# Performance work log

Hardware: AMD Instinct MI355X
Metric: run time of the kernel (lower is better)

Reference implementation:

```python
import jax, jax.numpy as jnp
import numpy as np

B, T, S, R, L = 16, 32, 512, 8, 256
H, E, V, NL = 512, 512, 50000, 3
OOV = 50


def setup_inputs() -> dict:
    key = jax.random.key(0)
    ks = jax.random.split(key, 40)
    p = lambda i, shape: jax.random.normal(ks[i], shape, dtype=jnp.float32) * 0.02
    d = {
        'tokens': jax.random.randint(ks[0], (B, T), 0, V),
        'src_oov': jax.random.randint(ks[1], (B, S), 0, V),
        'ref_oovs': jax.random.randint(ks[2], (B, R, L), 0, V),
        'src_mask': jnp.ones((B, S), bool),
        'ref_word_mask': jnp.ones((B, R, L), bool),
        'ref_doc_mask': jnp.ones((B, R), bool),
        'max_num_oov': OOV,
        'cur_word_rep': jax.random.normal(ks[3], (B, S, H), dtype=jnp.float32),
        'ref_word_reps': jax.random.normal(ks[4], (B, R, L, H), dtype=jnp.float32),
        'ref_doc_reps': jax.random.normal(ks[5], (B, R, H), dtype=jnp.float32),
        'hidden0': jax.random.normal(ks[6], (NL, B, H), dtype=jnp.float32),
        'embed_w': p(7, (V, E)),
        'gru_wih': p(8, (NL, 3 * H, H)),  # layer0 input dim E == H
        'gru_whh': p(9, (NL, 3 * H, H)),
        'gru_bih': p(10, (NL, 3 * H)),
        'gru_bhh': p(11, (NL, 3 * H)),
        'attn_Wd': p(12, (H, H)), 'attn_We': p(13, (H, H)), 'attn_v': p(14, (H,)),
        'hd_Wd': p(15, (H, H)), 'hd_We': p(16, (H, H)), 'hd_v': p(17, (H,)),
        'hw_Wd': p(18, (H, H)), 'hw_We': p(19, (H, H)), 'hw_v': p(20, (H,)),
        'gate_w': p(21, (2 * H, 1)), 'gate_b': p(22, (1,)),
        'fc_w': p(23, (2 * H, H)), 'fc_b': p(24, (H,)),
        'out_w': p(25, (H, V)), 'out_b': p(26, (V,)),
        'pgen_w': p(27, (E + 2 * H, 3)), 'pgen_b': p(28, (3,)),
    }
    return d


def _forward(embed_w, gru_wih, gru_whh, gru_bih, gru_bhh,
             attn_Wd, attn_We, attn_v, hd_Wd, hd_We, hd_v, hw_Wd, hw_We, hw_v,
             gate_w, gate_b, fc_w, fc_b, out_w, out_b, pgen_w, pgen_b,
             cur_word_rep, ref_word_reps, ref_doc_reps, hidden0,
             tokens, src_oov, ref_oovs, src_mask, ref_word_mask, ref_doc_mask,
             max_num_oov):
    b, t = tokens.shape
    x = embed_w[tokens]                               # [B,T,E]
    enc_proj = cur_word_rep @ attn_We                 # [B,S,H]
    doc_proj = ref_doc_reps @ hd_We                   # [B,R,H]
    word_proj = ref_word_reps @ hw_We                 # [B,R,L,H]
    NEG = jnp.float32(-1e9)

    def step(hidden, x_t):
        inp = x_t
        hs = []
        for l in range(hidden.shape[0]):
            gx = inp @ gru_wih[l].T + gru_bih[l]
            gh = hidden[l] @ gru_whh[l].T + gru_bhh[l]
            xr, xz, xn = jnp.split(gx, 3, -1)
            hr, hz, hn = jnp.split(gh, 3, -1)
            r = jax.nn.sigmoid(xr + hr)
            z = jax.nn.sigmoid(xz + hz)
            n = jnp.tanh(xn + r * hn)
            h = (1.0 - z) * n + z * hidden[l]
            hs.append(h)
            inp = h
        new_hidden = jnp.stack(hs)
        h_top = hs[-1]                                # [B,H]
        # additive attention over source words
        sc = jnp.tanh(enc_proj + (h_top @ attn_Wd)[:, None, :]) @ attn_v  # [B,S]
        aw = jax.nn.softmax(jnp.where(src_mask, sc, NEG), -1)
        ctx = jnp.einsum('bs,bsh->bh', aw, cur_word_rep)
        # hierarchical attention: doc level then word level
        scd = jnp.tanh(doc_proj + (h_top @ hd_Wd)[:, None, :]) @ hd_v     # [B,R]
        ad = jax.nn.softmax(jnp.where(ref_doc_mask, scd, NEG), -1)
        scw = jnp.tanh(word_proj + (h_top @ hw_Wd)[:, None, None, :]) @ hw_v  # [B,R,L]
        aww = jax.nn.softmax(jnp.where(ref_word_mask, scw, NEG), -1)
        ra = ad[:, :, None] * aww                     # [B,R,L]
        rctx = jnp.einsum('brl,brlh->bh', ra, ref_word_reps)
        # fusion gate
        g = jax.nn.sigmoid(jnp.concatenate([ctx, rctx], -1) @ gate_w + gate_b)  # [B,1]
        context = g * ctx + (1.0 - g) * rctx
        return new_hidden, (context, h_top, aw, ra)

    _, (contexts, hiddens, attn_dists, ref_attn_dists) = jax.lax.scan(
        step, hidden0, jnp.swapaxes(x, 0, 1))
    contexts = jnp.swapaxes(contexts, 0, 1)           # [B,T,H]
    hiddens = jnp.swapaxes(hiddens, 0, 1)             # [B,T,H]
    attn_dists = jnp.swapaxes(attn_dists, 0, 1)       # [B,T,S]
    ref_attn_dists = jnp.swapaxes(ref_attn_dists, 0, 1)  # [B,T,R,L]

    ch = jnp.concatenate([contexts, hiddens], -1)
    vocab_dist = jax.nn.softmax((ch @ fc_w + fc_b) @ out_w + out_b, -1)  # [B,T,V]
    pg = jax.nn.softmax(jnp.concatenate([contexts, hiddens, x], -1) @ pgen_w + pgen_b, -1)  # [B,T,3]
    vocab_dist_ = pg[..., 0:1] * vocab_dist
    attn_ = pg[..., 1:2] * attn_dists
    final = jnp.concatenate(
        [vocab_dist_, jnp.zeros((b, t, max_num_oov), vocab_dist_.dtype)], -1)
    bi = jnp.arange(b)[:, None, None]
    ti = jnp.arange(t)[None, :, None]
    idx = jnp.broadcast_to(src_oov[:, None, :], (b, t, src_oov.shape[-1]))
    final = final.at[bi, ti, idx].add(attn_)
    # multi-doc copy
    r, l = ref_oovs.shape[1], ref_oovs.shape[2]
    ref_attn_ = pg[..., 2][:, :, None, None] * ref_attn_dists
    ridx = jnp.broadcast_to(ref_oovs.reshape(b, 1, r * l), (b, t, r * l))
    final = final.at[bi, ti, ridx].add(ref_attn_.reshape(b, t, r * l))
    return final, attn_dists


def reference(tokens, src_oov, ref_oovs, src_mask, ref_word_mask, ref_doc_mask,
              max_num_oov, cur_word_rep, ref_word_reps, ref_doc_reps, hidden0,
              embed_w, gru_wih, gru_whh, gru_bih, gru_bhh,
              attn_Wd, attn_We, attn_v, hd_Wd, hd_We, hd_v, hw_Wd, hw_We, hw_v,
              gate_w, gate_b, fc_w, fc_b, out_w, out_b, pgen_w, pgen_b):
    return _forward(embed_w, gru_wih, gru_whh, gru_bih, gru_bhh,
                    attn_Wd, attn_We, attn_v, hd_Wd, hd_We, hd_v,
                    hw_Wd, hw_We, hw_v, gate_w, gate_b, fc_w, fc_b,
                    out_w, out_b, pgen_w, pgen_b,
                    cur_word_rep, ref_word_reps, ref_doc_reps, hidden0,
                    tokens, src_oov, ref_oovs, src_mask, ref_word_mask,
                    ref_doc_mask, max_num_oov)
```

## Files before the change

kernel.cpp:

```cpp
#include <hip/hip_runtime.h>
#include <hip/hip_bf16.h>


#define B_   16
#define T_   32
#define S_   512
#define R_   8
#define L_   256
#define RL_  2048
#define H_   512
#define V_   50000
#define NL_  3
#define OOV_ 50
#define M_   512
#define FINW 50050
#define S2C  2.8853900817779268f
#define GRUB 128
#define NCONV 128
#define HP16 520

typedef __attribute__((ext_vector_type(8))) short    short8;
typedef __attribute__((ext_vector_type(4))) float    f32x4;
typedef __attribute__((ext_vector_type(2))) _Float16 h2;
typedef __attribute__((ext_vector_type(8))) _Float16 h8;
typedef unsigned short u16;
typedef unsigned int   u32;
typedef unsigned long long u64;

#if __has_builtin(__builtin_amdgcn_exp2f)
#define EXP2F __builtin_amdgcn_exp2f
#else
#define EXP2F exp2f
#endif
#if __has_builtin(__builtin_amdgcn_rcpf)
#define RCPF __builtin_amdgcn_rcpf
#else
#define RCPF(x) (1.f/(x))
#endif

__device__ __forceinline__ float bf2f(u16 u){
  union { u32 i; float f; } v; v.i = ((u32)u) << 16; return v.f;
}
__device__ __forceinline__ u16 f2bf(float f){
  union { float f; u32 i; } v; v.f = f;
  return (u16)((v.i + 0x7FFFu + ((v.i >> 16) & 1u)) >> 16);
}
__device__ __forceinline__ u16 f2h(float f){
  union { _Float16 h; u16 u; } v; v.h = (_Float16)f; return v.u;
}
__device__ __forceinline__ float tanh_(float x){
  float e = __expf(2.f * x);
  return 1.f - 2.f / (e + 1.f);
}
__device__ __forceinline__ float sigmoid_(float x){
  return 1.f / (1.f + __expf(-x));
}
__device__ __forceinline__ float dot8h(h8 w, h8 x, float acc){
#if __has_builtin(__builtin_amdgcn_fdot2)
  acc = __builtin_amdgcn_fdot2((h2){w[0], w[1]}, (h2){x[0], x[1]}, acc, false);
  acc = __builtin_amdgcn_fdot2((h2){w[2], w[3]}, (h2){x[2], x[3]}, acc, false);
  acc = __builtin_amdgcn_fdot2((h2){w[4], w[5]}, (h2){x[4], x[5]}, acc, false);
  acc = __builtin_amdgcn_fdot2((h2){w[6], w[7]}, (h2){x[6], x[7]}, acc, false);
#else
  #pragma unroll
  for (int q = 0; q < 8; q++) acc += (float)w[q] * (float)x[q];
#endif
  return acc;
}
__device__ __forceinline__ u64 allc(const u64* p){
  return __hip_atomic_load(p, __ATOMIC_RELAXED, __HIP_MEMORY_SCOPE_AGENT);
}
__device__ __forceinline__ float allcf(const float* p){
  u32 v = __hip_atomic_load((const u32*)p, __ATOMIC_RELAXED, __HIP_MEMORY_SCOPE_AGENT);
  union { u32 i; float f; } c; c.i = v; return c.f;
}


__global__ __launch_bounds__(256) void k_embed(const int* __restrict__ tokens,
                                               const float* __restrict__ embed_w,
                                               u16* __restrict__ x_bf){
  int rid = blockIdx.x;
  long tok = (long)tokens[rid];
  const float* src = embed_w + tok * H_;
  u16* dst = x_bf + (long)rid * H_;
  for (int e = threadIdx.x; e < H_; e += 256) dst[e] = f2bf(src[e]);
}

struct CJ { const float* s; u16* d; long n; int f16; };

__global__ __launch_bounds__(256) void k_conv6(CJ j0, CJ j1, CJ j2, CJ j3, CJ j4, CJ j5){
  int y = blockIdx.y;
  CJ j = (y == 0) ? j0 : (y == 1) ? j1 : (y == 2) ? j2 : (y == 3) ? j3 : (y == 4) ? j4 : j5;
  long n4 = j.n >> 2;
  long i = (long)blockIdx.x * 256 + threadIdx.x;
  long stride = (long)gridDim.x * 256;
  if (j.f16){
    for (; i < n4; i += stride){
      f32x4 v = *(const f32x4*)(j.s + 4 * i);
      u64 p = (u64)f2h(v[0]) | ((u64)f2h(v[1]) << 16)
            | ((u64)f2h(v[2]) << 32) | ((u64)f2h(v[3]) << 48);
      *(u64*)(j.d + 4 * i) = p;
    }
  } else {
    for (; i < n4; i += stride){
      f32x4 v = *(const f32x4*)(j.s + 4 * i);
      u64 p = (u64)f2bf(v[0]) | ((u64)f2bf(v[1]) << 16)
            | ((u64)f2bf(v[2]) << 32) | ((u64)f2bf(v[3]) << 48);
      *(u64*)(j.d + 4 * i) = p;
    }
  }
}

__global__ __launch_bounds__(256) void k_convT(const float* __restrict__ src, int Rr, int Cc,
                                               u16* __restrict__ dst){
  __shared__ float tile[32][33];
  int c0 = blockIdx.x * 32, r0 = blockIdx.y * 32;
  int tx = threadIdx.x & 31, ty = threadIdx.x >> 5;
  for (int i = ty; i < 32; i += 8){
    int r = r0 + i, c = c0 + tx;
    tile[i][tx] = (r < Rr && c < Cc) ? src[(long)r * Cc + c] : 0.f;
  }
  __syncthreads();
  for (int i = ty; i < 32; i += 8){
    int c = c0 + i, r = r0 + tx;
    if (c < Cc && r < Rr) dst[(long)c * Rr + r] = f2bf(tile[tx][i]);
  }
}

__global__ __launch_bounds__(256) void k_convT6(const float* s0, const float* s1,
    const float* s2, const float* s3, const float* s4, const float* s5,
    u16* __restrict__ dstb){
  int z = blockIdx.z;
  const float* src = (z == 0) ? s0 : (z == 1) ? s1 : (z == 2) ? s2
                   : (z == 3) ? s3 : (z == 4) ? s4 : s5;
  u16* dst = dstb + (long)z * H_ * H_;
  __shared__ float tile[32][33];
  int c0 = blockIdx.x * 32, r0 = blockIdx.y * 32;
  int tx = threadIdx.x & 31, ty = threadIdx.x >> 5;
  for (int i = ty; i < 32; i += 8)
    tile[i][tx] = src[(long)(r0 + i) * H_ + c0 + tx];
  __syncthreads();
  for (int i = ty; i < 32; i += 8)
    dst[(long)(c0 + i) * H_ + r0 + tx] = f2bf(tile[tx][i]);
}


__device__ void dev_gemm_tile(const u16* __restrict__ A, int lda,
                              const u16* __restrict__ W, int ldw,
                              const float* __restrict__ bias,
                              void* __restrict__ Cv, long ldc,
                              int N, int K, int c_bf16, float cscale,
                              int bx, int by, int t256){
  int wave = t256 >> 6, lane = t256 & 63;
  int m0 = bx * 128 + (wave >> 1) * 64;
  int n0 = by * 128 + (wave & 1) * 64;
  int lr = lane & 15, lk = (lane >> 4) * 8;
  f32x4 acc[4][4];
  #pragma unroll
  for (int i = 0; i < 4; i++)
    #pragma unroll
    for (int j = 0; j < 4; j++) acc[i][j] = (f32x4){0.f, 0.f, 0.f, 0.f};

  short8 a0[4], b0[4];
  #pragma unroll
  for (int i = 0; i < 4; i++)
    a0[i] = *(const short8*)(A + (long)(m0 + i * 16 + lr) * lda + lk);
  #pragma unroll
  for (int j = 0; j < 4; j++){
    int c = n0 + j * 16 + lr;
    b0[j] = (c < N) ? *(const short8*)(W + (long)c * ldw + lk) : (short8){0,0,0,0,0,0,0,0};
  }
  for (int k0 = 0; k0 < K; k0 += 32){
    short8 a1[4], b1[4];
    if (k0 + 32 < K){
      int kn = k0 + 32 + lk;
      #pragma unroll
      for (int i = 0; i < 4; i++)
        a1[i] = *(const short8*)(A + (long)(m0 + i * 16 + lr) * lda + kn);
      #pragma unroll
      for (int j = 0; j < 4; j++){
        int c = n0 + j * 16 + lr;
        b1[j] = (c < N) ? *(const short8*)(W + (long)c * ldw + kn) : (short8){0,0,0,0,0,0,0,0};
      }
    }
    #pragma unroll
    for (int i = 0; i < 4; i++)
      #pragma unroll
      for (int j = 0; j < 4; j++)
        acc[i][j] = __builtin_amdgcn_mfma_f32_16x16x32_bf16(a0[i], b0[j], acc[i][j], 0, 0, 0);
    #pragma unroll
    for (int i = 0; i < 4; i++) a0[i] = a1[i];
    #pragma unroll
    for (int j = 0; j < 4; j++) b0[j] = b1[j];
  }
  int rr = (lane >> 4) * 4;
  #pragma unroll
  for (int j = 0; j < 4; j++){
    int c = n0 + j * 16 + lr;
    if (c >= N) continue;
    float bv = bias ? bias[c] : 0.f;
    #pragma unroll
    for (int i = 0; i < 4; i++){
      #pragma unroll
      for (int e = 0; e < 4; e++){
        long r = m0 + i * 16 + rr + e;
        float v = fmaf(acc[i][j][e], cscale, bv);
        if (c_bf16) ((u16*)Cv)[r * ldc + c] = f2bf(v);
        else        ((float*)Cv)[r * ldc + c] = v;
      }
    }
  }
}

__global__ __launch_bounds__(256) void k_gemm_nt(const u16* __restrict__ A, int lda,
                                                 const u16* __restrict__ W, int ldw,
                                                 const float* __restrict__ bias,
                                                 void* __restrict__ Cv, long ldc,
                                                 int N, int K, int c_bf16, float cscale){
  dev_gemm_tile(A, lda, W, ldw, bias, Cv, ldc, N, K, c_bf16, cscale,
                blockIdx.x, blockIdx.y, threadIdx.x);
}


__global__ __launch_bounds__(256) void k_gemm_out(const u16* __restrict__ A,
    const u16* __restrict__ W, const float* __restrict__ bias,
    float* __restrict__ fin, float* __restrict__ pm, float* __restrict__ ps){
  const int N = V_;
  __shared__ float cbuf[128][132];
  __shared__ float smx[128][2], ssx[128][2];
  int tid = threadIdx.x;
  int wave = tid >> 6, lane = tid & 63;
  int mb = blockIdx.x * 128, nb = blockIdx.y * 128;
  int m0 = mb + (wave >> 1) * 64;
  int n0 = nb + (wave & 1) * 64;
  int lr = lane & 15, lk = (lane >> 4) * 8;
  f32x4 acc[4][4];
  #pragma unroll
  for (int i = 0; i < 4; i++)
    #pragma unroll
    for (int j = 0; j < 4; j++) acc[i][j] = (f32x4){0.f, 0.f, 0.f, 0.f};

  short8 a0[4], b0[4];
  #pragma unroll
  for (int i = 0; i < 4; i++)
    a0[i] = *(const short8*)(A + (long)(m0 + i * 16 + lr) * 512 + lk);
  #pragma unroll
  for (int j = 0; j < 4; j++){
    int c = n0 + j * 16 + lr;
    b0[j] = (c < N) ? *(const short8*)(W + (long)c * 512 + lk) : (short8){0,0,0,0,0,0,0,0};
  }
  for (int k0 = 0; k0 < 512; k0 += 32){
    short8 a1[4], b1[4];
    if (k0 + 32 < 512){
      int kn = k0 + 32 + lk;
      #pragma unroll
      for (int i = 0; i < 4; i++)
        a1[i] = *(const short8*)(A + (long)(m0 + i * 16 + lr) * 512 + kn);
      #pragma unroll
      for (int j = 0; j < 4; j++){
        int c = n0 + j * 16 + lr;
        b1[j] = (c < N) ? *(const short8*)(W + (long)c * 512 + kn) : (short8){0,0,0,0,0,0,0,0};
      }
    }
    #pragma unroll
    for (int i = 0; i < 4; i++)
      #pragma unroll
      for (int j = 0; j < 4; j++)
        acc[i][j] = __builtin_amdgcn_mfma_f32_16x16x32_bf16(a0[i], b0[j], acc[i][j], 0, 0, 0);
    #pragma unroll
    for (int i = 0; i < 4; i++) a0[i] = a1[i];
    #pragma unroll
    for (int j = 0; j < 4; j++) b0[j] = b1[j];
  }
  int rr = (lane >> 4) * 4;
  int rloc0 = (wave >> 1) * 64, cloc0 = (wave & 1) * 64;
  #pragma unroll
  for (int j = 0; j < 4; j++){
    int c = n0 + j * 16 + lr;
    float bv = (c < N) ? bias[c] : 0.f;
    #pragma unroll
    for (int i = 0; i < 4; i++){
      #pragma unroll
      for (int e = 0; e < 4; e++)
        cbuf[rloc0 + i * 16 + rr + e][cloc0 + j * 16 + lr] = acc[i][j][e] + bv;
    }
  }
  __syncthreads();
  int rl = tid >> 1, ch = tid & 1;
  int cbase = ch * 64;
  int cg = nb + cbase;
  long gbase = (long)(mb + rl) * FINW + cg;
  float mp = -1e30f;
  #pragma unroll 8
  for (int k = 0; k < 64; k += 2){
    float x0 = cbuf[rl][cbase + k], x1 = cbuf[rl][cbase + k + 1];
    float2 xy; xy.x = x0; xy.y = x1;
    *(float2*)(fin + gbase + k) = xy;
    if (cg + k < N)     mp = fmaxf(mp, x0);
    if (cg + k + 1 < N) mp = fmaxf(mp, x1);
  }
  float sp = 0.f;
  #pragma unroll 8
  for (int k = 0; k < 64; k++){
    if (cg + k < N) sp += __expf(cbuf[rl][cbase + k] - mp);
  }
  smx[rl][ch] = mp; ssx[rl][ch] = sp;
  __syncthreads();
  if (tid < 128){
    float ma = smx[tid][0], mb2 = smx[tid][1];
    float M = fmaxf(ma, mb2);
    float S = ssx[tid][0] * __expf(ma - M) + ssx[tid][1] * __expf(mb2 - M);
    long row = mb + tid;
    pm[row * 392 + blockIdx.y] = M;
    ps[row * 392 + blockIdx.y] = S;
  }
}


__global__ __launch_bounds__(512) void k_gru_mega(
    const float* __restrict__ gx0, const u16* __restrict__ wih_h,
    const u16* __restrict__ whh_h, const float* __restrict__ bih,
    const float* __restrict__ bhh, const float* __restrict__ hidden0,
    float* __restrict__ h_all, u16* __restrict__ ch_bf, unsigned int* cnt,
    const float* __restrict__ out_w, u16* __restrict__ outwT,
    const u16* __restrict__ cwr_bf, const u16* __restrict__ rwr_bf,
    const u16* __restrict__ rdr_bf, const u16* __restrict__ WT,
    u16* __restrict__ enc_bf, u16* __restrict__ wp_bf,
    float* __restrict__ doc_proj, int do_shadow){
  __shared__ u16 pH0[16][HP16], pH1[16][HP16], pX1[16][HP16], pH2[16][HP16], pX2[16][HP16];
  __shared__ float red0[8][3][4][16];
  __shared__ float red1[8][6][4][16];
  __shared__ float red2[8][6][4][16];
  __shared__ float tconv[2][32][33];
  int bid = blockIdx.x;
  int tid = threadIdx.x;

  if (bid >= GRUB){
    if (!do_shadow) return;
    int wid = bid - GRUB;
    int half = tid >> 8, t256 = tid & 255;
    int worker = wid * 2 + half;
    for (int tile = worker; tile < 1284; tile += 256){
      if (tile < 256)
        dev_gemm_tile(cwr_bf, H_, WT, H_, (const float*)0, (void*)enc_bf, H_,
                      H_, H_, 1, S2C, tile >> 2, tile & 3, t256);
      else if (tile < 1280){
        int t = tile - 256;
        dev_gemm_tile(rwr_bf, H_, WT + 2 * H_ * H_, H_, (const float*)0, (void*)wp_bf, H_,
                      H_, H_, 1, S2C, t >> 2, t & 3, t256);
      } else
        dev_gemm_tile(rdr_bf, H_, WT + H_ * H_, H_, (const float*)0, (void*)doc_proj, H_,
                      H_, H_, 0, S2C, 0, tile - 1280, t256);
    }
    __syncthreads();
    int sub = half, tx = t256 & 31, ty = t256 >> 5;
    const int NT = 1563 * 16;
    for (int base = wid * 2; base < NT; base += NCONV * 2){
      int tile = base + sub;
      bool act = tile < NT;
      int cx = act ? (tile % 1563) : 0;
      int ry = act ? (tile / 1563) : 0;
      int c0 = cx * 32, r0 = ry * 32;
      if (act){
        for (int i = ty; i < 32; i += 8){
          int c = c0 + tx;
          tconv[sub][i][tx] = (c < V_) ? out_w[(long)(r0 + i) * V_ + c] : 0.f;
        }
      }
      __syncthreads();
      if (act){
        for (int i = ty; i < 32; i += 8){
          int c = c0 + i;
          if (c < V_) outwT[(long)c * H_ + r0 + tx] = f2bf(tconv[sub][tx][i]);
        }
      }
      __syncthreads();
    }
    return;
  }

  int bx = bid;
  int b = tid & 15, jj = (tid >> 4) & 3, ks = tid >> 6;
  int j = bx * 4 + jj;
  int kbase = ks * 64;
  int srow = tid >> 5, sl32 = tid & 31;

  for (int s = 0; s < T_ + NL_ - 1; s++){
    int t0 = s, t1 = s - 1, t2v = s - 2;
    bool a0 = (t0 < T_);
    bool a1 = (t1 >= 0 && t1 < T_);
    bool a2 = (t2v >= 0 && t2v < T_);
    float hpj_r = 0.f, gx_r0 = 0.f, gx_r1 = 0.f, gx_r2 = 0.f;
    if (tid < 192){
      int lz = tid >> 6, b2 = tid & 15, jj2 = (tid >> 4) & 3;
      int j2 = bx * 4 + jj2;
      int tt = s - lz;
      if (tt >= 0 && tt < T_){
        hpj_r = (tt == 0) ? hidden0[(lz * B_ + b2) * H_ + j2]
                          : allcf(h_all + (long)((lz * T_ + tt - 1) * B_ + b2) * H_ + j2);
        if (lz == 0){
          const float* g = gx0 + (long)(b2 * T_ + tt) * 1536 + j2;
          gx_r0 = g[0]; gx_r1 = g[512]; gx_r2 = g[1024];
        }
      }
    }
    {
      u64 v;
      #define STAGE(PAN, ROWPTR, ATOMIC)                                         \
        {                                                                        \
          const u64* p = (const u64*)(ROWPTR);                                   \
          _Pragma("unroll")                                                      \
          for (int q = 0; q < 8; q++){                                           \
            v = (ATOMIC) ? allc(p + sl32 + 32 * q) : p[sl32 + 32 * q];           \
            union { u64 w; float f[2]; } uu; uu.w = v;                           \
            union { _Float16 h[2]; u32 u; } pk;                                  \
            pk.h[0] = (_Float16)uu.f[0]; pk.h[1] = (_Float16)uu.f[1];            \
            *(u32*)&PAN[srow][2 * (sl32 + 32 * q)] = pk.u;                       \
          }                                                                      \
        }
      if (a0){
        if (t0 == 0) STAGE(pH0, hidden0 + (long)(0 * B_ + srow) * H_, false)
        else         STAGE(pH0, h_all + (long)((0 * T_ + t0 - 1) * B_ + srow) * H_, true)
      }
      if (a1){
        if (t1 == 0) STAGE(pH1, hidden0 + (long)(1 * B_ + srow) * H_, false)
        else         STAGE(pH1, h_all + (long)((1 * T_ + t1 - 1) * B_ + srow) * H_, true)
        STAGE(pX1, h_all + (long)((0 * T_ + t1) * B_ + srow) * H_, true)
      }
      if (a2){
        if (t2v == 0) STAGE(pH2, hidden0 + (long)(2 * B_ + srow) * H_, false)
        else          STAGE(pH2, h_all + (long)((2 * T_ + t2v - 1) * B_ + srow) * H_, true)
        STAGE(pX2, h_all + (long)((1 * T_ + t2v) * B_ + srow) * H_, true)
      }
      #undef STAGE
    }
    __syncthreads();

    if (a0){
      const u16* wl = whh_h;
      const h8* w0 = (const h8*)(wl + ((long)(0 * H_ + j)) * H_ + kbase);
      const h8* w1 = (const h8*)(wl + ((long)(1 * H_ + j)) * H_ + kbase);
      const h8* w2 = (const h8*)(wl + ((long)(2 * H_ + j)) * H_ + kbase);
      float s0 = 0.f, s1 = 0.f, s2 = 0.f;
      #pragma unroll 2
      for (int k8 = 0; k8 < 8; k8++){
        h8 hv = *(const h8*)&pH0[b][kbase + 8 * k8];
        s0 = dot8h(w0[k8], hv, s0);
        s1 = dot8h(w1[k8], hv, s1);
        s2 = dot8h(w2[k8], hv, s2);
      }
      red0[ks][0][jj][b] = s0; red0[ks][1][jj][b] = s1; red0[ks][2][jj][b] = s2;
    }
    if (a1){
      const u16* wl = whh_h + (long)1 * 1536 * H_;
      const u16* ul = wih_h + (long)1 * 1536 * H_;
      const h8* w0 = (const h8*)(wl + ((long)(0 * H_ + j)) * H_ + kbase);
      const h8* w1 = (const h8*)(wl + ((long)(1 * H_ + j)) * H_ + kbase);
      const h8* w2 = (const h8*)(wl + ((long)(2 * H_ + j)) * H_ + kbase);
      const h8* u0 = (const h8*)(ul + ((long)(0 * H_ + j)) * H_ + kbase);
      const h8* u1 = (const h8*)(ul + ((long)(1 * H_ + j)) * H_ + kbase);
      const h8* u2 = (const h8*)(ul + ((long)(2 * H_ + j)) * H_ + kbase);
      float s0 = 0.f, s1 = 0.f, s2 = 0.f, x0 = 0.f, x1 = 0.f, x2 = 0.f;
      #pragma unroll 2
      for (int k8 = 0; k8 < 8; k8++){
        h8 hv = *(const h8*)&pH1[b][kbase + 8 * k8];
        h8 xv = *(const h8*)&pX1[b][kbase + 8 * k8];
        s0 = dot8h(w0[k8], hv, s0);
        s1 = dot8h(w1[k8], hv, s1);
        s2 = dot8h(w2[k8], hv, s2);
        x0 = dot8h(u0[k8], xv, x0);
        x1 = dot8h(u1[k8], xv, x1);
        x2 = dot8h(u2[k8], xv, x2);
      }
      red1[ks][0][jj][b] = s0; red1[ks][1][jj][b] = s1; red1[ks][2][jj][b] = s2;
      red1[ks][3][jj][b] = x0; red1[ks][4][jj][b] = x1; red1[ks][5][jj][b] = x2;
    }
    if (a2){
      const u16* wl = whh_h + (long)2 * 1536 * H_;
      const u16* ul = wih_h + (long)2 * 1536 * H_;
      const h8* w0 = (const h8*)(wl + ((long)(0 * H_ + j)) * H_ + kbase);
      const h8* w1 = (const h8*)(wl + ((long)(1 * H_ + j)) * H_ + kbase);
      const h8* w2 = (const h8*)(wl + ((long)(2 * H_ + j)) * H_ + kbase);
      const h8* u0 = (const h8*)(ul + ((long)(0 * H_ + j)) * H_ + kbase);
      const h8* u1 = (const h8*)(ul + ((long)(1 * H_ + j)) * H_ + kbase);
      const h8* u2 = (const h8*)(ul + ((long)(2 * H_ + j)) * H_ + kbase);
      float s0 = 0.f, s1 = 0.f, s2 = 0.f, x0 = 0.f, x1 = 0.f, x2 = 0.f;
      #pragma unroll 2
      for (int k8 = 0; k8 < 8; k8++){
        h8 hv = *(const h8*)&pH2[b][kbase + 8 * k8];
        h8 xv = *(const h8*)&pX2[b][kbase + 8 * k8];
        s0 = dot8h(w0[k8], hv, s0);
        s1 = dot8h(w1[k8], hv, s1);
        s2 = dot8h(w2[k8], hv, s2);
        x0 = dot8h(u0[k8], xv, x0);
        x1 = dot8h(u1[k8], xv, x1);
        x2 = dot8h(u2[k8], xv, x2);
      }
      red2[ks][0][jj][b] = s0; red2[ks][1][jj][b] = s1; red2[ks][2][jj][b] = s2;
      red2[ks][3][jj][b] = x0; red2[ks][4][jj][b] = x1; red2[ks][5][jj][b] = x2;
    }
    __syncthreads();

    if (tid < 192){
      int lz = tid >> 6, b2 = tid & 15, jj2 = (tid >> 4) & 3;
      int j2 = bx * 4 + jj2;
      int tt = s - lz;
      if (tt >= 0 && tt < T_){
        float gh[3], gxv[3];
        #pragma unroll
        for (int g = 0; g < 3; g++){
          float a = 0.f, c = 0.f;
          if (lz == 0){
            #pragma unroll
            for (int q = 0; q < 8; q++) a += red0[q][g][jj2][b2];
          } else if (lz == 1){
            #pragma unroll
            for (int q = 0; q < 8; q++){ a += red1[q][g][jj2][b2]; c += red1[q][3 + g][jj2][b2]; }
          } else {
            #pragma unroll
            for (int q = 0; q < 8; q++){ a += red2[q][g][jj2][b2]; c += red2[q][3 + g][jj2][b2]; }
          }
          gh[g] = a + bhh[lz * 1536 + g * H_ + j2];
          if (lz == 0) gxv[g] = (g == 0) ? gx_r0 : (g == 1) ? gx_r1 : gx_r2;
          else         gxv[g] = c + bih[lz * 1536 + g * H_ + j2];
        }
        float r = sigmoid_(gxv[0] + gh[0]);
        float z = sigmoid_(gxv[1] + gh[1]);
        float n = tanh_(gxv[2] + r * gh[2]);
        float h = (1.f - z) * n + z * hpj_r;
        union { float f; u32 u; } cv; cv.f = h;
        __hip_atomic_store((u32*)(h_all + (long)((lz * T_ + tt) * B_ + b2) * H_ + j2),
                           cv.u, __ATOMIC_RELAXED, __HIP_MEMORY_SCOPE_AGENT);
        if (lz == 2) ch_bf[(long)(b2 * T_ + tt) * 1024 + 512 + j2] = f2bf(h);
      }
    }
    if (s == T_ + NL_ - 2) break;

    __syncthreads();
    if (tid == 0)
      __hip_atomic_store(cnt + bx * 16, (u32)(s + 1),
                         __ATOMIC_RELAXED, __HIP_MEMORY_SCOPE_AGENT);
    if (tid < GRUB){
      long guard = 0;
      while (__hip_atomic_load(cnt + tid * 16, __ATOMIC_RELAXED, __HIP_MEMORY_SCOPE_AGENT)
               < (u32)(s + 1) && guard < (1L << 23)){
        __builtin_amdgcn_s_sleep(1);
        guard++;
      }
    }
    __syncthreads();
  }
}


__global__ __launch_bounds__(256) void k_scores2(const u16* __restrict__ enc,
    const u16* __restrict__ wp, const float* __restrict__ dec_all,
    const float* __restrict__ av, const float* __restrict__ wv,
    float* __restrict__ aw, float* __restrict__ ra){
  int b = blockIdx.x, y = blockIdx.y, tz = blockIdx.z;
  const u16* ebf; int erpb, doff, et, ldo; const float* vv; float* out;
  if (y < 8){ ebf = enc; erpb = S_;  doff = 0;    vv = av; out = aw; ldo = S_;  et = y; }
  else      { ebf = wp;  erpb = RL_; doff = 1024; vv = wv; out = ra; ldo = RL_; et = y - 8; }
  int tid = threadIdx.x;
  __shared__ float dsh[8][512];
  __shared__ float vsh[512];
  __shared__ float redsv[4];
  for (int i = tid; i < 8 * 128; i += 256){
    int tl = i >> 7, c = (i & 127) << 2;
    *(f32x4*)&dsh[tl][c] =
      *(const f32x4*)(dec_all + ((long)(b * T_) + tz * 8 + tl) * 1536 + doff + c);
  }
  for (int i = tid; i < 128; i += 256)
    *(f32x4*)&vsh[i << 2] = *(const f32x4*)(vv + (i << 2));
  __syncthreads();
  float pvv = vsh[tid] + vsh[tid + 256];
  for (int o = 32; o > 0; o >>= 1) pvv += __shfl_xor(pvv, o);
  if ((tid & 63) == 0) redsv[tid >> 6] = pvv;
  __syncthreads();
  float sumv = redsv[0] + redsv[1] + redsv[2] + redsv[3];

  int el = tid & 63, tq = tid >> 6;
  const u16* erow = ebf + ((long)b * erpb + et * 64 + el) * H_;
  float acc0 = 0.f, acc1 = 0.f;
  for (int h0 = 0; h0 < H_; h0 += 8){
    short8 ev = *(const short8*)(erow + h0);
    float w[8], vq[8];
    #pragma unroll
    for (int q = 0; q < 8; q++) w[q] = bf2f((u16)ev[q]);
    #pragma unroll
    for (int q = 0; q < 8; q++) vq[q] = vsh[h0 + q];
    const float* d0 = &dsh[tq * 2 + 0][h0];
    const float* d1 = &dsh[tq * 2 + 1][h0];
    #pragma unroll
    for (int q = 0; q < 8; q++){
      float e0 = EXP2F(w[q] + d0[q]);
      acc0 += vq[q] * RCPF(e0 + 1.f);
      float e1 = EXP2F(w[q] + d1[q]);
      acc1 += vq[q] * RCPF(e1 + 1.f);
    }
  }
  int eg = et * 64 + el;
  long r0 = (long)(b * T_ + tz * 8 + tq * 2 + 0) * ldo + eg;
  long r1 = (long)(b * T_ + tz * 8 + tq * 2 + 1) * ldo + eg;
  out[r0] = sumv - 2.f * acc0;
  out[r1] = sumv - 2.f * acc1;
}


__global__ __launch_bounds__(256) void k_smax_scd(float* __restrict__ aw,
    const float* __restrict__ doc_proj, const float* __restrict__ dec_all,
    const float* __restrict__ hd_v, float* __restrict__ ad){
  int rid = blockIdx.x, tid = threadIdx.x;
  __shared__ float red4[4];
  __shared__ float red8[8][32];
  if (blockIdx.y == 0){
    float* row = aw + (long)rid * S_;
    float x0 = row[tid], x1 = row[tid + 256];
    float m = fmaxf(x0, x1);
    for (int o = 32; o > 0; o >>= 1) m = fmaxf(m, __shfl_xor(m, o));
    if ((tid & 63) == 0) red4[tid >> 6] = m;
    __syncthreads();
    m = fmaxf(fmaxf(red4[0], red4[1]), fmaxf(red4[2], red4[3]));
    float e0 = __expf(x0 - m), e1 = __expf(x1 - m);
    float s = e0 + e1;
    for (int o = 32; o > 0; o >>= 1) s += __shfl_xor(s, o);
    __syncthreads();
    if ((tid & 63) == 0) red4[tid >> 6] = s;
    __syncthreads();
    s = red4[0] + red4[1] + red4[2] + red4[3];
    float inv = 1.f / s;
    row[tid] = e0 * inv; row[tid + 256] = e1 * inv;
  } else {
    int b = rid / T_;
    int r = tid >> 5, kp = tid & 31;
    const float* dp = doc_proj + (long)(b * R_ + r) * H_;
    const float* d  = dec_all + (long)rid * 1536 + 512;
    float s = 0.f;
    for (int h = kp * 16; h < kp * 16 + 16; h++){
      float e = EXP2F(dp[h] + d[h]);
      s += hd_v[h] * (1.f - 2.f * RCPF(e + 1.f));
    }
    red8[r][kp] = s;
    __syncthreads();
    if (tid < 8){
      float sc = 0.f;
      for (int k = 0; k < 32; k++) sc += red8[tid][k];
      red8[tid][0] = sc;
    }
    __syncthreads();
    if (tid == 0){
      float m = -1e30f;
      for (int q = 0; q < 8; q++) m = fmaxf(m, red8[q][0]);
      float e[8], sum = 0.f;
      for (int q = 0; q < 8; q++){ e[q] = __expf(red8[q][0] - m); sum += e[q]; }
      float inv = 1.f / sum;
      for (int q = 0; q < 8; q++) ad[rid * R_ + q] = e[q] * inv;
    }
  }
}

__global__ __launch_bounds__(256) void k_aww_ra(float* __restrict__ raBuf,
                                                const float* __restrict__ ad){
  int rid = blockIdx.x, r = blockIdx.y, tid = threadIdx.x;
  float* row = raBuf + (long)rid * RL_ + r * L_;
  float x = row[tid];
  float m = x;
  for (int o = 32; o > 0; o >>= 1) m = fmaxf(m, __shfl_xor(m, o));
  __shared__ float red[4];
  if ((tid & 63) == 0) red[tid >> 6] = m;
  __syncthreads();
  m = fmaxf(fmaxf(red[0], red[1]), fmaxf(red[2], red[3]));
  float e = __expf(x - m);
  float s = e;
  for (int o = 32; o > 0; o >>= 1) s += __shfl_xor(s, o);
  __syncthreads();
  if ((tid & 63) == 0) red[tid >> 6] = s;
  __syncthreads();
  s = red[0] + red[1] + red[2] + red[3];
  row[tid] = (e / s) * ad[rid * R_ + r];
}


__global__ __launch_bounds__(256) void k_awgemm(const float* __restrict__ wts, int KS, int CH,
    const u16* __restrict__ Wbuf, float* __restrict__ pdst){
  int b = blockIdx.x, ht = blockIdx.y, kc = blockIdx.z;
  int tid = threadIdx.x;
  int hl = tid & 63, tq = tid >> 6;
  int h = ht * 256 + hl * 4;
  int base = kc * CH;
  float a[8][4];
  #pragma unroll
  for (int tt = 0; tt < 8; tt++)
    #pragma unroll
    for (int q = 0; q < 4; q++) a[tt][q] = 0.f;
  const float* wrow = wts + ((long)(b * T_) + tq * 8) * KS + base;
  for (int sl = 0; sl < CH; sl++){
    const u16* wp = Wbuf + ((long)b * KS + base + sl) * H_ + h;
    u32 p0 = *(const u32*)(wp);
    u32 p1 = *(const u32*)(wp + 2);
    float v0 = bf2f((u16)(p0 & 0xffff)), v1 = bf2f((u16)(p0 >> 16));
    float v2 = bf2f((u16)(p1 & 0xffff)), v3 = bf2f((u16)(p1 >> 16));
    #pragma unroll
    for (int tt = 0; tt < 8; tt++){
      float w = wrow[(long)tt * KS + sl];
      a[tt][0] += w * v0; a[tt][1] += w * v1;
      a[tt][2] += w * v2; a[tt][3] += w * v3;
    }
  }
  #pragma unroll
  for (int tt = 0; tt < 8; tt++){
    long o = (long)kc * (2 * M_ * H_) + ((long)(b * T_ + tq * 8 + tt)) * H_ + h;
    *(f32x4*)(pdst + o) = (f32x4){a[tt][0], a[tt][1], a[tt][2], a[tt][3]};
  }
}

__global__ __launch_bounds__(256) void k_red8(const float* __restrict__ pbuf,
                                              float* __restrict__ outp){
  long n = 2L * M_ * H_;
  long i = (long)blockIdx.x * 256 + threadIdx.x;
  if (i >= n) return;
  float s = 0.f;
  #pragma unroll
  for (int kc = 0; kc < 8; kc++) s += pbuf[(long)kc * n + i];
  outp[i] = s;
}


__global__ __launch_bounds__(256) void k_gatepgen(const float* __restrict__ ctx,
    const float* __restrict__ rctx, const float* __restrict__ gate_w,
    const float* __restrict__ gate_b, float* __restrict__ contexts,
    u16* __restrict__ ch_bf, const float* __restrict__ h_all,
    const u16* __restrict__ x_bf, const float* __restrict__ pgen_w,
    const float* __restrict__ pgen_b, float* __restrict__ pg){
  int rid = blockIdx.x, tid = threadIdx.x;
  int b = rid / T_, t = rid % T_;
  const float* c  = ctx  + (long)rid * H_;
  const float* rc = rctx + (long)rid * H_;
  float part = 0.f;
  for (int h = tid; h < H_; h += 256) part += c[h] * gate_w[h] + rc[h] * gate_w[H_ + h];
  for (int o = 32; o > 0; o >>= 1) part += __shfl_xor(part, o);
  __shared__ float red[4];
  if ((tid & 63) == 0) red[tid >> 6] = part;
  __syncthreads();
  float g = sigmoid_(red[0] + red[1] + red[2] + red[3] + gate_b[0]);
  for (int h = tid; h < H_; h += 256){
    float v = g * c[h] + (1.f - g) * rc[h];
    contexts[(long)rid * H_ + h] = v;
    ch_bf[(long)rid * 1024 + h] = f2bf(v);
  }
  float p0 = 0.f, p1 = 0.f, p2 = 0.f;
  for (int k = tid; k < 1536; k += 256){
    float v;
    if (k < 512)       v = g * c[k] + (1.f - g) * rc[k];
    else if (k < 1024) v = h_all[((2 * T_ + t) * B_ + b) * H_ + (k - 512)];
    else               v = bf2f(x_bf[(long)rid * H_ + (k - 1024)]);
    p0 += v * pgen_w[k * 3 + 0];
    p1 += v * pgen_w[k * 3 + 1];
    p2 += v * pgen_w[k * 3 + 2];
  }
  for (int o = 32; o > 0; o >>= 1){
    p0 += __shfl_xor(p0, o); p1 += __shfl_xor(p1, o); p2 += __shfl_xor(p2, o);
  }
  __shared__ float r0[4], r1[4], r2[4];
  if ((tid & 63) == 0){ r0[tid >> 6] = p0; r1[tid >> 6] = p1; r2[tid >> 6] = p2; }
  __syncthreads();
  if (tid == 0){
    p0 = r0[0]+r0[1]+r0[2]+r0[3] + pgen_b[0];
    p1 = r1[0]+r1[1]+r1[2]+r1[3] + pgen_b[1];
    p2 = r2[0]+r2[1]+r2[2]+r2[3] + pgen_b[2];
    float m = fmaxf(p0, fmaxf(p1, p2));
    float e0 = __expf(p0 - m), e1 = __expf(p1 - m), e2 = __expf(p2 - m);
    float inv = 1.f / (e0 + e1 + e2);
    pg[rid * 3 + 0] = e0 * inv;
    pg[rid * 3 + 1] = e1 * inv;
    pg[rid * 3 + 2] = e2 * inv;
  }
}


__global__ __launch_bounds__(256) void k_vred391(const float* __restrict__ pm,
    const float* __restrict__ ps, float* __restrict__ vmax, float* __restrict__ vsum){
  int rid = blockIdx.x, tid = threadIdx.x;
  const float* mrow = pm + (long)rid * 392;
  const float* srow = ps + (long)rid * 392;
  float m = -1e30f, s = 0.f;
  for (int q = tid; q < 391; q += 256){
    float m2 = mrow[q], s2 = srow[q];
    float M = fmaxf(m, m2);
    s = s * __expf(m - M) + s2 * __expf(m2 - M);
    m = M;
  }
  for (int o = 32; o > 0; o >>= 1){
    float m2 = __shfl_xor(m, o), s2 = __shfl_xor(s, o);
    float M = fmaxf(m, m2);
    s = s * __expf(m - M) + s2 * __expf(m2 - M);
    m = M;
  }
  __shared__ float rm[4], rs[4];
  if ((tid & 63) == 0){ rm[tid >> 6] = m; rs[tid >> 6] = s; }
  __syncthreads();
  if (tid == 0){
    float Mx = rm[0], Sx = rs[0];
    for (int q = 1; q < 4; q++){
      float M2 = fmaxf(Mx, rm[q]);
      Sx = Sx * __expf(Mx - M2) + rs[q] * __expf(rm[q] - M2);
      Mx = M2;
    }
    vmax[rid] = Mx; vsum[rid] = Sx;
  }
}

__global__ __launch_bounds__(256) void k_final_vocab(float* __restrict__ fin,
    const float* __restrict__ vmax, const float* __restrict__ vsum,
    const float* __restrict__ pg){
  int rid = blockIdx.y;
  int v = (blockIdx.x * 256 + threadIdx.x) * 2;
  if (v >= FINW) return;
  long base = (long)rid * FINW;
  float scale = pg[rid * 3 + 0] / vsum[rid];
  float mx = vmax[rid];
  if (v + 1 < V_){
    float2* p = (float2*)(fin + base + v);
    float2 x = *p;
    x.x = __expf(x.x - mx) * scale;
    x.y = __expf(x.y - mx) * scale;
    *p = x;
  } else {
    for (int q = 0; q < 2 && v + q < FINW; q++){
      float x = fin[base + v + q];
      fin[base + v + q] = (v + q < V_) ? __expf(x - mx) * scale : 0.f;
    }
  }
}

__global__ __launch_bounds__(256) void k_scatter_src(float* __restrict__ fin,
    const float* __restrict__ aw, const float* __restrict__ pg,
    const int* __restrict__ src_oov){
  int rid = blockIdx.x, tid = threadIdx.x;
  int b = rid / T_;
  float p1 = pg[rid * 3 + 1];
  for (int s = tid; s < S_; s += 256){
    float val = p1 * aw[(long)rid * S_ + s];
    int idx = src_oov[b * S_ + s];
    atomicAdd(fin + (long)rid * FINW + idx, val);
  }
}

__global__ __launch_bounds__(256) void k_scatter_ref(float* __restrict__ fin,
    const float* __restrict__ raBuf, const float* __restrict__ pg,
    const int* __restrict__ ref_oovs){
  int rid = blockIdx.x, tid = threadIdx.x;
  int b = rid / T_;
  float p2 = pg[rid * 3 + 2];
  for (int i = tid; i < RL_; i += 256){
    float val = p2 * raBuf[(long)rid * RL_ + i];
    int idx = ref_oovs[b * RL_ + i];
    atomicAdd(fin + (long)rid * FINW + idx, val);
  }
}


extern "C" void kernel_launch(void* const* d_in, const int* in_sizes, int n_in,
                              void* d_out, int out_size, void* d_ws, size_t ws_size,
                              hipStream_t stream)
{
  (void)in_sizes; (void)n_in; (void)out_size;
  const int*   tokens   = (const int*)  d_in[0];
  const int*   src_oov  = (const int*)  d_in[1];
  const int*   ref_oovs = (const int*)  d_in[2];
  const float* cwr      = (const float*)d_in[7];
  const float* rwr      = (const float*)d_in[8];
  const float* rdr      = (const float*)d_in[9];
  const float* hidden0  = (const float*)d_in[10];
  const float* embed_w  = (const float*)d_in[11];
  const float* gru_wih  = (const float*)d_in[12];
  const float* gru_whh  = (const float*)d_in[13];
  const float* gru_bih  = (const float*)d_in[14];
  const float* gru_bhh  = (const float*)d_in[15];
  const float* attn_Wd  = (const float*)d_in[16];
  const float* attn_We  = (const float*)d_in[17];
  const float* attn_v   = (const float*)d_in[18];
  const float* hd_Wd    = (const float*)d_in[19];
  const float* hd_We    = (const float*)d_in[20];
  const float* hd_v     = (const float*)d_in[21];
  const float* hw_Wd    = (const float*)d_in[22];
  const float* hw_We    = (const float*)d_in[23];
  const float* hw_v     = (const float*)d_in[24];
  const float* gate_w   = (const float*)d_in[25];
  const float* gate_b   = (const float*)d_in[26];
  const float* fc_w     = (const float*)d_in[27];
  const float* fc_b     = (const float*)d_in[28];
  const float* out_w    = (const float*)d_in[29];
  const float* out_b    = (const float*)d_in[30];
  const float* pgen_w   = (const float*)d_in[31];
  const float* pgen_b   = (const float*)d_in[32];

  float* fin = (float*)d_out;
  float* aw  = fin + (long)M_ * FINW;

  char* wptr = (char*)d_ws;
  auto alloc = [&](size_t nbytes) -> void* {
    void* p = (void*)wptr;
    wptr += (nbytes + 255) & ~(size_t)255;
    return p;
  };
  float* gx0      = (float*)alloc((size_t)M_ * 1536 * 4);
  float* h_all    = (float*)alloc((size_t)NL_ * T_ * B_ * H_ * 4);
  float* dec_all  = (float*)alloc((size_t)M_ * 1536 * 4);
  float* raBuf    = (float*)alloc((size_t)M_ * RL_ * 4);
  float* ad       = (float*)alloc((size_t)M_ * R_ * 4);
  float* ctx      = (float*)alloc((size_t)M_ * H_ * 4);
  float* rctx     = (float*)alloc((size_t)M_ * H_ * 4);
  float* contexts = (float*)alloc((size_t)M_ * H_ * 4);
  float* pg       = (float*)alloc((size_t)M_ * 3 * 4);
  float* vmax     = (float*)alloc((size_t)M_ * 4);
  float* vsum     = (float*)alloc((size_t)M_ * 4);
  float* pm       = (float*)alloc((size_t)M_ * 392 * 4);
  float* ps       = (float*)alloc((size_t)M_ * 392 * 4);
  float* doc_proj = (float*)alloc((size_t)B_ * R_ * H_ * 4);
  float* pbuf     = (float*)alloc((size_t)8 * 2 * M_ * H_ * 4);
  unsigned int* gru_cnt = (unsigned int*)alloc(GRUB * 16 * 4);
  u16* x_bf       = (u16*)alloc((size_t)M_ * H_ * 2);
  u16* ch_bf      = (u16*)alloc((size_t)M_ * 1024 * 2);
  u16* whh_h16    = (u16*)alloc((size_t)NL_ * 1536 * H_ * 2);
  u16* wih_h16    = (u16*)alloc((size_t)NL_ * 1536 * H_ * 2);
  u16* wih0_bf    = (u16*)alloc((size_t)1536 * H_ * 2);
  u16* WT         = (u16*)alloc((size_t)6 * H_ * H_ * 2);
  u16* fcwT       = (u16*)alloc((size_t)H_ * 1024 * 2);
  u16* fcout_bf   = (u16*)alloc((size_t)M_ * H_ * 2);
  u16* cwr_bf     = (u16*)alloc((size_t)B_ * S_ * H_ * 2);
  u16* enc_bf     = (u16*)alloc((size_t)B_ * S_ * H_ * 2);
  u16* rwr_bf     = (u16*)alloc((size_t)B_ * RL_ * H_ * 2);
  u16* wp_bf      = (u16*)alloc((size_t)B_ * RL_ * H_ * 2);
  u16* rdr_bf     = (u16*)alloc((size_t)B_ * R_ * H_ * 2);
  u16* outwT_ded  = (u16*)alloc((size_t)V_ * H_ * 2);
  bool big = ((char*)outwT_ded + (size_t)V_ * H_ * 2) <= ((char*)d_ws + ws_size);
  u16* outwT = big ? outwT_ded : rwr_bf;
  int nshadow = big ? NCONV : 0;

  hipMemsetAsync(gru_cnt, 0, GRUB * 16 * 4, stream);

  k_embed<<<M_, 256, 0, stream>>>(tokens, embed_w, x_bf);
  {
    CJ j0{cwr, cwr_bf, (long)B_ * S_ * H_, 0};
    CJ j1{rwr, rwr_bf, (long)B_ * RL_ * H_, 0};
    CJ j2{gru_whh, whh_h16, (long)NL_ * 1536 * H_, 1};
    CJ j3{gru_wih, wih_h16, (long)NL_ * 1536 * H_, 1};
    CJ j4{rdr, rdr_bf, (long)B_ * R_ * H_, 0};
    CJ j5{gru_wih, wih0_bf, (long)1536 * H_, 0};
    k_conv6<<<dim3(512, 6), 256, 0, stream>>>(j0, j1, j2, j3, j4, j5);
  }
  k_convT6<<<dim3(16, 16, 6), 256, 0, stream>>>(attn_We, hd_We, hw_We,
                                                attn_Wd, hd_Wd, hw_Wd, WT);
  k_convT<<<dim3(16, 32), 256, 0, stream>>>(fc_w, 1024, H_, fcwT);

  k_gemm_nt<<<dim3(4, 12), 256, 0, stream>>>(x_bf, H_, wih0_bf, H_, gru_bih,
                                             (void*)gx0, 1536, 1536, H_, 0, 1.f);
  if (!big){
    k_gemm_nt<<<dim3(64, 4), 256, 0, stream>>>(cwr_bf, H_, WT, H_, (const float*)0,
                                               (void*)enc_bf, H_, H_, H_, 1, S2C);
    k_gemm_nt<<<dim3(256, 4), 256, 0, stream>>>(rwr_bf, H_, WT + 2 * H_ * H_, H_, (const float*)0,
                                                (void*)wp_bf, H_, H_, H_, 1, S2C);
    k_gemm_nt<<<dim3(1, 4), 256, 0, stream>>>(rdr_bf, H_, WT + H_ * H_, H_, (const float*)0,
                                              (void*)doc_proj, H_, H_, H_, 0, S2C);
  }

  k_gru_mega<<<GRUB + nshadow, 512, 0, stream>>>(gx0, wih_h16, whh_h16, gru_bih, gru_bhh,
                                                 hidden0, h_all, ch_bf, gru_cnt,
                                                 out_w, outwT, cwr_bf, rwr_bf, rdr_bf,
                                                 WT, enc_bf, wp_bf, doc_proj, big ? 1 : 0);

  k_gemm_nt<<<dim3(4, 12), 256, 0, stream>>>(ch_bf + 512, 1024, WT + 3 * H_ * H_, H_,
                                             (const float*)0, (void*)dec_all, 1536, 1536, H_, 0, S2C);

  k_scores2<<<dim3(16, 40, 4), 256, 0, stream>>>(enc_bf, wp_bf, dec_all, attn_v, hw_v, aw, raBuf);
  k_smax_scd<<<dim3(M_, 2), 256, 0, stream>>>(aw, doc_proj, dec_all, hd_v, ad);
  k_aww_ra<<<dim3(M_, R_), 256, 0, stream>>>(raBuf, ad);

  k_awgemm<<<dim3(B_, 2, 8), 256, 0, stream>>>(aw, S_, 64, cwr_bf, pbuf);
  k_awgemm<<<dim3(B_, 2, 8), 256, 0, stream>>>(raBuf, RL_, 256, rwr_bf, pbuf + (long)M_ * H_);
  if (!big)
    k_convT<<<dim3(1563, 16), 256, 0, stream>>>(out_w, H_, V_, outwT);
  k_red8<<<(2 * M_ * H_ + 255) / 256, 256, 0, stream>>>(pbuf, ctx);

  k_gatepgen<<<M_, 256, 0, stream>>>(ctx, rctx, gate_w, gate_b, contexts, ch_bf,
                                     h_all, x_bf, pgen_w, pgen_b, pg);

  k_gemm_nt<<<dim3(4, 4), 256, 0, stream>>>(ch_bf, 1024, fcwT, 1024, fc_b,
                                            (void*)fcout_bf, H_, H_, 1024, 1, 1.f);
  k_gemm_out<<<dim3(4, 391), 256, 0, stream>>>(fcout_bf, outwT, out_b, fin, pm, ps);
  k_vred391<<<M_, 256, 0, stream>>>(pm, ps, vmax, vsum);
  k_final_vocab<<<dim3(98, M_), 256, 0, stream>>>(fin, vmax, vsum, pg);
  k_scatter_src<<<M_, 256, 0, stream>>>(fin, aw, pg, src_oov);
  k_scatter_ref<<<M_, 256, 0, stream>>>(fin, raBuf, pg, ref_oovs);
}
```

Measured before the change: 1.148 ms.

## Fuse tail kernels and share GRU staging panels across layers

Merges the two attention-weighted GEMM launches into one grid, folds the 391-way softmax reduction into the final vocab kernel (each block recomputes the row max/sum), and combines the two copy scatters into one 512-thread kernel. In the GRU megakernel, the adjacent layers' staged hidden states are shared, so layer l's input panel reuses layer l-1's hidden panel, cutting LDS staging traffic and shared-memory footprint. The goal is fewer launches and less redundant global/LDS loads; the cost is redundant per-block softmax reductions (98x per row). The counter buffer is also enlarged without apparent use.

```diff
diff --git a/kernel.cpp b/kernel.cpp
--- a/kernel.cpp
+++ b/kernel.cpp
@@ -327,7 +327,7 @@
     const u16* __restrict__ rdr_bf, const u16* __restrict__ WT,
     u16* __restrict__ enc_bf, u16* __restrict__ wp_bf,
     float* __restrict__ doc_proj, int do_shadow){
-  __shared__ u16 pH0[16][HP16], pH1[16][HP16], pX1[16][HP16], pH2[16][HP16], pX2[16][HP16];
+  __shared__ u16 P0[16][HP16], P1[16][HP16], P2[16][HP16];
   __shared__ float red0[8][3][4][16];
   __shared__ float red1[8][6][4][16];
   __shared__ float red2[8][6][4][16];
@@ -418,19 +418,13 @@
             *(u32*)&PAN[srow][2 * (sl32 + 32 * q)] = pk.u;                       \
           }                                                                      \
         }
-      if (a0){
-        if (t0 == 0) STAGE(pH0, hidden0 + (long)(0 * B_ + srow) * H_, false)
-        else         STAGE(pH0, h_all + (long)((0 * T_ + t0 - 1) * B_ + srow) * H_, true)
-      }
-      if (a1){
-        if (t1 == 0) STAGE(pH1, hidden0 + (long)(1 * B_ + srow) * H_, false)
-        else         STAGE(pH1, h_all + (long)((1 * T_ + t1 - 1) * B_ + srow) * H_, true)
-        STAGE(pX1, h_all + (long)((0 * T_ + t1) * B_ + srow) * H_, true)
-      }
+      if (a0 && t0 == 0)      STAGE(P0, hidden0 + (long)(0 * B_ + srow) * H_, false)
+      else if (a0 || a1)      STAGE(P0, h_all + (long)((0 * T_ + s - 1) * B_ + srow) * H_, true)
+      if (a1 && t1 == 0)      STAGE(P1, hidden0 + (long)(1 * B_ + srow) * H_, false)
+      else if (a1 || a2)      STAGE(P1, h_all + (long)((1 * T_ + s - 2) * B_ + srow) * H_, true)
       if (a2){
-        if (t2v == 0) STAGE(pH2, hidden0 + (long)(2 * B_ + srow) * H_, false)
-        else          STAGE(pH2, h_all + (long)((2 * T_ + t2v - 1) * B_ + srow) * H_, true)
-        STAGE(pX2, h_all + (long)((1 * T_ + t2v) * B_ + srow) * H_, true)
+        if (t2v == 0)         STAGE(P2, hidden0 + (long)(2 * B_ + srow) * H_, false)
+        else                  STAGE(P2, h_all + (long)((2 * T_ + s - 3) * B_ + srow) * H_, true)
       }
       #undef STAGE
     }
@@ -444,7 +438,7 @@
       float s0 = 0.f, s1 = 0.f, s2 = 0.f;
       #pragma unroll 2
       for (int k8 = 0; k8 < 8; k8++){
-        h8 hv = *(const h8*)&pH0[b][kbase + 8 * k8];
+        h8 hv = *(const h8*)&P0[b][kbase + 8 * k8];
         s0 = dot8h(w0[k8], hv, s0);
         s1 = dot8h(w1[k8], hv, s1);
         s2 = dot8h(w2[k8], hv, s2);
@@ -463,8 +457,8 @@
       float s0 = 0.f, s1 = 0.f, s2 = 0.f, x0 = 0.f, x1 = 0.f, x2 = 0.f;
       #pragma unroll 2
       for (int k8 = 0; k8 < 8; k8++){
-        h8 hv = *(const h8*)&pH1[b][kbase + 8 * k8];
-        h8 xv = *(const h8*)&pX1[b][kbase + 8 * k8];
+        h8 hv = *(const h8*)&P1[b][kbase + 8 * k8];
+        h8 xv = *(const h8*)&P0[b][kbase + 8 * k8];
         s0 = dot8h(w0[k8], hv, s0);
         s1 = dot8h(w1[k8], hv, s1);
         s2 = dot8h(w2[k8], hv, s2);
@@ -487,8 +481,8 @@
       float s0 = 0.f, s1 = 0.f, s2 = 0.f, x0 = 0.f, x1 = 0.f, x2 = 0.f;
       #pragma unroll 2
       for (int k8 = 0; k8 < 8; k8++){
-        h8 hv = *(const h8*)&pH2[b][kbase + 8 * k8];
-        h8 xv = *(const h8*)&pX2[b][kbase + 8 * k8];
+        h8 hv = *(const h8*)&P2[b][kbase + 8 * k8];
+        h8 xv = *(const h8*)&P1[b][kbase + 8 * k8];
         s0 = dot8h(w0[k8], hv, s0);
         s1 = dot8h(w1[k8], hv, s1);
         s2 = dot8h(w2[k8], hv, s2);
@@ -681,9 +675,13 @@
 }
 
 
-__global__ __launch_bounds__(256) void k_awgemm(const float* __restrict__ wts, int KS, int CH,
-    const u16* __restrict__ Wbuf, float* __restrict__ pdst){
-  int b = blockIdx.x, ht = blockIdx.y, kc = blockIdx.z;
+__global__ __launch_bounds__(256) void k_awgemm2(const float* __restrict__ aw,
+    const float* __restrict__ raBuf, const u16* __restrict__ cwr_bf,
+    const u16* __restrict__ rwr_bf, float* __restrict__ pbuf){
+  int b = blockIdx.x, ht = blockIdx.y, z = blockIdx.z;
+  const float* wts; const u16* Wbuf; float* pdst; int KS, CH, kc;
+  if (z < 8){ wts = aw;    Wbuf = cwr_bf; pdst = pbuf;                 KS = S_;  CH = 64;  kc = z; }
+  else      { wts = raBuf; Wbuf = rwr_bf; pdst = pbuf + (long)M_ * H_; KS = RL_; CH = 256; kc = z - 8; }
   int tid = threadIdx.x;
   int hl = tid & 63, tq = tid >> 6;
   int h = ht * 256 + hl * 4;
@@ -778,9 +776,10 @@
 }
 
 
-__global__ __launch_bounds__(256) void k_vred391(const float* __restrict__ pm,
-    const float* __restrict__ ps, float* __restrict__ vmax, float* __restrict__ vsum){
-  int rid = blockIdx.x, tid = threadIdx.x;
+__global__ __launch_bounds__(256) void k_final_vocab(float* __restrict__ fin,
+    const float* __restrict__ pm, const float* __restrict__ ps,
+    const float* __restrict__ pg){
+  int rid = blockIdx.y, tid = threadIdx.x;
   const float* mrow = pm + (long)rid * 392;
   const float* srow = ps + (long)rid * 392;
   float m = -1e30f, s = 0.f;
@@ -796,7 +795,7 @@
     s = s * __expf(m - M) + s2 * __expf(m2 - M);
     m = M;
   }
-  __shared__ float rm[4], rs[4];
+  __shared__ float rm[4], rs[4], fm, fs;
   if ((tid & 63) == 0){ rm[tid >> 6] = m; rs[tid >> 6] = s; }
   __syncthreads();
   if (tid == 0){
@@ -806,19 +805,14 @@
       Sx = Sx * __expf(Mx - M2) + rs[q] * __expf(rm[q] - M2);
       Mx = M2;
     }
-    vmax[rid] = Mx; vsum[rid] = Sx;
-  }
-}
-
-__global__ __launch_bounds__(256) void k_final_vocab(float* __restrict__ fin,
-    const float* __restrict__ vmax, const float* __restrict__ vsum,
-    const float* __restrict__ pg){
-  int rid = blockIdx.y;
-  int v = (blockIdx.x * 256 + threadIdx.x) * 2;
+    fm = Mx; fs = Sx;
+  }
+  __syncthreads();
+  float mx = fm;
+  float scale = pg[rid * 3 + 0] / fs;
+  int v = (blockIdx.x * 256 + tid) * 2;
   if (v >= FINW) return;
   long base = (long)rid * FINW;
-  float scale = pg[rid * 3 + 0] / vsum[rid];
-  float mx = vmax[rid];
   if (v + 1 < V_){
     float2* p = (float2*)(fin + base + v);
     float2 x = *p;
@@ -833,29 +827,27 @@
   }
 }
 
-__global__ __launch_bounds__(256) void k_scatter_src(float* __restrict__ fin,
-    const float* __restrict__ aw, const float* __restrict__ pg,
-    const int* __restrict__ src_oov){
-  int rid = blockIdx.x, tid = threadIdx.x;
-  int b = rid / T_;
-  float p1 = pg[rid * 3 + 1];
-  for (int s = tid; s < S_; s += 256){
-    float val = p1 * aw[(long)rid * S_ + s];
-    int idx = src_oov[b * S_ + s];
-    atomicAdd(fin + (long)rid * FINW + idx, val);
-  }
-}
-
-__global__ __launch_bounds__(256) void k_scatter_ref(float* __restrict__ fin,
-    const float* __restrict__ raBuf, const float* __restrict__ pg,
+__global__ __launch_bounds__(512) void k_scatter(float* __restrict__ fin,
+    const float* __restrict__ aw, const float* __restrict__ raBuf,
+    const float* __restrict__ pg, const int* __restrict__ src_oov,
     const int* __restrict__ ref_oovs){
   int rid = blockIdx.x, tid = threadIdx.x;
   int b = rid / T_;
-  float p2 = pg[rid * 3 + 2];
-  for (int i = tid; i < RL_; i += 256){
-    float val = p2 * raBuf[(long)rid * RL_ + i];
-    int idx = ref_oovs[b * RL_ + i];
-    atomicAdd(fin + (long)rid * FINW + idx, val);
+  if (tid < 256){
+    float p1 = pg[rid * 3 + 1];
+    for (int s = tid; s < S_; s += 256){
+      float val = p1 * aw[(long)rid * S_ + s];
+      int idx = src_oov[b * S_ + s];
+      atomicAdd(fin + (long)rid * FINW + idx, val);
+    }
+  } else {
+    int t2 = tid - 256;
+    float p2 = pg[rid * 3 + 2];
+    for (int i = t2; i < RL_; i += 256){
+      float val = p2 * raBuf[(long)rid * RL_ + i];
+      int idx = ref_oovs[b * RL_ + i];
+      atomicAdd(fin + (long)rid * FINW + idx, val);
+    }
   }
 }
 
@@ -913,13 +905,11 @@
   float* rctx     = (float*)alloc((size_t)M_ * H_ * 4);
   float* contexts = (float*)alloc((size_t)M_ * H_ * 4);
   float* pg       = (float*)alloc((size_t)M_ * 3 * 4);
-  float* vmax     = (float*)alloc((size_t)M_ * 4);
-  float* vsum     = (float*)alloc((size_t)M_ * 4);
   float* pm       = (float*)alloc((size_t)M_ * 392 * 4);
   float* ps       = (float*)alloc((size_t)M_ * 392 * 4);
   float* doc_proj = (float*)alloc((size_t)B_ * R_ * H_ * 4);
   float* pbuf     = (float*)alloc((size_t)8 * 2 * M_ * H_ * 4);
-  unsigned int* gru_cnt = (unsigned int*)alloc(GRUB * 16 * 4);
+  unsigned int* gru_cnt = (unsigned int*)alloc((GRUB + NCONV) * 16 * 4);
   u16* x_bf       = (u16*)alloc((size_t)M_ * H_ * 2);
   u16* ch_bf      = (u16*)alloc((size_t)M_ * 1024 * 2);
   u16* whh_h16    = (u16*)alloc((size_t)NL_ * 1536 * H_ * 2);
@@ -938,7 +928,7 @@
   u16* outwT = big ? outwT_ded : rwr_bf;
   int nshadow = big ? NCONV : 0;
 
-  hipMemsetAsync(gru_cnt, 0, GRUB * 16 * 4, stream);
+  hipMemsetAsync(gru_cnt, 0, (GRUB + NCONV) * 16 * 4, stream);
 
   k_embed<<<M_, 256, 0, stream>>>(tokens, embed_w, x_bf);
   {
@@ -977,8 +967,7 @@
   k_smax_scd<<<dim3(M_, 2), 256, 0, stream>>>(aw, doc_proj, dec_all, hd_v, ad);
   k_aww_ra<<<dim3(M_, R_), 256, 0, stream>>>(raBuf, ad);
 
-  k_awgemm<<<dim3(B_, 2, 8), 256, 0, stream>>>(aw, S_, 64, cwr_bf, pbuf);
-  k_awgemm<<<dim3(B_, 2, 8), 256, 0, stream>>>(raBuf, RL_, 256, rwr_bf, pbuf + (long)M_ * H_);
+  k_awgemm2<<<dim3(B_, 2, 16), 256, 0, stream>>>(aw, raBuf, cwr_bf, rwr_bf, pbuf);
   if (!big)
     k_convT<<<dim3(1563, 16), 256, 0, stream>>>(out_w, H_, V_, outwT);
   k_red8<<<(2 * M_ * H_ + 255) / 256, 256, 0, stream>>>(pbuf, ctx);
@@ -989,8 +978,6 @@
   k_gemm_nt<<<dim3(4, 4), 256, 0, stream>>>(ch_bf, 1024, fcwT, 1024, fc_b,
                                             (void*)fcout_bf, H_, H_, 1024, 1, 1.f);
   k_gemm_out<<<dim3(4, 391), 256, 0, stream>>>(fcout_bf, outwT, out_b, fin, pm, ps);
-  k_vred391<<<M_, 256, 0, stream>>>(pm, ps, vmax, vsum);
-  k_final_vocab<<<dim3(98, M_), 256, 0, stream>>>(fin, vmax, vsum, pg);
-  k_scatter_src<<<M_, 256, 0, stream>>>(fin, aw, pg, src_oov);
-  k_scatter_ref<<<M_, 256, 0, stream>>>(fin, raBuf, pg, ref_oovs);
-}
+  k_final_vocab<<<dim3(98, M_), 256, 0, stream>>>(fin, pm, ps, pg);
+  k_scatter<<<M_, 512, 0, stream>>>(fin, aw, raBuf, pg, src_oov, ref_oovs);
+}
```

New measurement: 1.120 ms, median of 2. 1.02x faster.
